# Performance work log

Measured on AMD Instinct MI355X. Metric: run time of the kernel, lower is better.

Reference implementation:

```python
import jax, jax.numpy as jnp
import numpy as np

B, S, RNN, ATTH = 256, 196, 1024, 512  # batch, att_size, rnn_size, att_h_size


def setup_inputs() -> dict:
    key = jax.random.key(0)
    k1, k2, k3, k4, k5, k6, k7 = jax.random.split(key, 7)
    h = jax.random.normal(k1, (B, RNN), dtype=jnp.float32)
    att_feats = jax.random.normal(k2, (B, S, RNN), dtype=jnp.float32)
    p_att_feats = jax.random.normal(k3, (B, S, ATTH), dtype=jnp.float32)
    # learned params (torch nn.Linear: y = x @ W.T + b)
    w_h2att = jax.random.normal(k4, (ATTH, RNN), dtype=jnp.float32) / np.sqrt(RNN)
    b_h2att = jax.random.normal(k5, (ATTH,), dtype=jnp.float32) * 0.01
    w_alpha = jax.random.normal(k6, (1, ATTH), dtype=jnp.float32) / np.sqrt(ATTH)
    b_alpha = jax.random.normal(k7, (1,), dtype=jnp.float32) * 0.01
    return {
        "h": h,
        "att_feats": att_feats,
        "p_att_feats": p_att_feats,
        "w_h2att": w_h2att,
        "b_h2att": b_h2att,
        "w_alpha": w_alpha,
        "b_alpha": b_alpha,
    }


def reference(h, att_feats, p_att_feats, w_h2att, b_h2att, w_alpha, b_alpha):
    # att_h = h2att(h): [B, ATTH]
    att_h = h @ w_h2att.T + b_h2att
    # additive combine + tanh: [B, S, ATTH]
    dot = jnp.tanh(p_att_feats + att_h[:, None, :])
    # alpha_net: [B, S]
    scores = jnp.einsum("bsa,a->bs", dot, w_alpha[0]) + b_alpha[0]
    weight = jax.nn.softmax(scores, axis=1)
    # weighted sum of att_feats: [B, RNN]
    att_res = jnp.einsum("bs,bsd->bd", weight, att_feats)
    return att_res
```

## Files before the change

### kernel.cpp

```cpp
#include <hip/hip_runtime.h>
#include <cstddef>

static constexpr int kB    = 256;
static constexpr int kS    = 196;
static constexpr int kRNN  = 1024;
static constexpr int kATTH = 512;

__device__ __forceinline__ float fast_tanh(float x) {
    x = fminf(12.0f, fmaxf(-12.0f, x));
    float e = __expf(2.0f * x);
    return __fdividef(e - 1.0f, e + 1.0f);
}

__global__ __launch_bounds__(256) void gemm_atth(
    const float* __restrict__ h, const float* __restrict__ w,
    const float* __restrict__ bias, float* __restrict__ att_h) {
    __shared__ float As[32][33];
    __shared__ float Bs[32][33];
    const int bm = blockIdx.x * 32;
    const int bn = blockIdx.y * 32;
    const int tid = threadIdx.x;
    const int lrow = tid >> 3;
    const int lcol = (tid & 7) << 2;
    const int tx = tid & 31;
    const int ty = tid >> 5;
    float acc[4] = {0.f, 0.f, 0.f, 0.f};
    for (int k0 = 0; k0 < kRNN; k0 += 32) {
        float4 av = *(const float4*)&h[(size_t)(bm + lrow) * kRNN + k0 + lcol];
        float4 bv = *(const float4*)&w[(size_t)(bn + lrow) * kRNN + k0 + lcol];
        As[lrow][lcol + 0] = av.x; As[lrow][lcol + 1] = av.y;
        As[lrow][lcol + 2] = av.z; As[lrow][lcol + 3] = av.w;
        Bs[lrow][lcol + 0] = bv.x; Bs[lrow][lcol + 1] = bv.y;
        Bs[lrow][lcol + 2] = bv.z; Bs[lrow][lcol + 3] = bv.w;
        __syncthreads();
#pragma unroll
        for (int k = 0; k < 32; ++k) {
            float bb = Bs[tx][k];
#pragma unroll
            for (int i = 0; i < 4; ++i) acc[i] += As[ty * 4 + i][k] * bb;
        }
        __syncthreads();
    }
    const float bval = bias[bn + tx];
#pragma unroll
    for (int i = 0; i < 4; ++i)
        att_h[(size_t)(bm + ty * 4 + i) * kATTH + bn + tx] = acc[i] + bval;
}

__global__ __launch_bounds__(1024) void att_fused(
    const float* __restrict__ att_feats, const float* __restrict__ p_att,
    const float* __restrict__ att_h, const float* __restrict__ w_alpha,
    const float* __restrict__ b_alpha, float* __restrict__ out) {
    const int b = blockIdx.x;
    const int tid = threadIdx.x;
    const int lane = tid & 63;
    const int wave = tid >> 6;

    __shared__ float sScore[kS];
    __shared__ float4 sRed[3][256];

    const int col = lane << 3;
    const float4 ah0 = *(const float4*)&att_h[(size_t)b * kATTH + col];
    const float4 ah1 = *(const float4*)&att_h[(size_t)b * kATTH + col + 4];
    const float4 wa0 = *(const float4*)&w_alpha[col];
    const float4 wa1 = *(const float4*)&w_alpha[col + 4];
    const float balpha = b_alpha[0];

    for (int s = wave; s < kS; s += 16) {
        const float* p = &p_att[((size_t)b * kS + s) * kATTH + col];
        const float4 p0 = *(const float4*)p;
        const float4 p1 = *(const float4*)(p + 4);
        float partial;
        partial  = fast_tanh(p0.x + ah0.x) * wa0.x;
        partial += fast_tanh(p0.y + ah0.y) * wa0.y;
        partial += fast_tanh(p0.z + ah0.z) * wa0.z;
        partial += fast_tanh(p0.w + ah0.w) * wa0.w;
        partial += fast_tanh(p1.x + ah1.x) * wa1.x;
        partial += fast_tanh(p1.y + ah1.y) * wa1.y;
        partial += fast_tanh(p1.z + ah1.z) * wa1.z;
        partial += fast_tanh(p1.w + ah1.w) * wa1.w;
#pragma unroll
        for (int off = 32; off > 0; off >>= 1)
            partial += __shfl_xor(partial, off, 64);
        if (lane == 0) sScore[s] = partial + balpha;
    }
    __syncthreads();

    if (tid < 64) {
        float vals[4];
        int cnt = 0;
        float m = -3.0e38f;
        for (int s = tid; s < kS; s += 64) {
            vals[cnt] = sScore[s];
            m = fmaxf(m, vals[cnt]);
            ++cnt;
        }
#pragma unroll
        for (int off = 32; off > 0; off >>= 1) m = fmaxf(m, __shfl_xor(m, off, 64));
        float sum = 0.f;
        for (int i = 0; i < cnt; ++i) { vals[i] = __expf(vals[i] - m); sum += vals[i]; }
#pragma unroll
        for (int off = 32; off > 0; off >>= 1) sum += __shfl_xor(sum, off, 64);
        const float inv = __fdividef(1.0f, sum);
        cnt = 0;
        for (int s = tid; s < kS; s += 64) { sScore[s] = vals[cnt] * inv; ++cnt; }
    }
    __syncthreads();

    const int d4 = tid & 255;
    const int sg = tid >> 8;
    float4 acc = {0.f, 0.f, 0.f, 0.f};
    for (int s = sg; s < kS; s += 4) {
        const float ws = sScore[s];
        const float4 v =
            *(const float4*)&att_feats[((size_t)b * kS + s) * kRNN + (d4 << 2)];
        acc.x += ws * v.x; acc.y += ws * v.y;
        acc.z += ws * v.z; acc.w += ws * v.w;
    }
    if (sg > 0) sRed[sg - 1][d4] = acc;
    __syncthreads();
    if (sg == 0) {
        const float4 r0 = sRed[0][d4];
        const float4 r1 = sRed[1][d4];
        const float4 r2 = sRed[2][d4];
        acc.x += r0.x + r1.x + r2.x;
        acc.y += r0.y + r1.y + r2.y;
        acc.z += r0.z + r1.z + r2.z;
        acc.w += r0.w + r1.w + r2.w;
        *(float4*)&out[(size_t)b * kRNN + (d4 << 2)] = acc;
    }
}

extern "C" void kernel_launch(void* const* d_in, const int* in_sizes, int n_in,
                              void* d_out, int out_size, void* d_ws, size_t ws_size,
                              hipStream_t stream) {
    const float* h         = (const float*)d_in[0];
    const float* att_feats = (const float*)d_in[1];
    const float* p_att     = (const float*)d_in[2];
    const float* w_h2att   = (const float*)d_in[3];
    const float* b_h2att   = (const float*)d_in[4];
    const float* w_alpha   = (const float*)d_in[5];
    const float* b_alpha   = (const float*)d_in[6];
    float* out = (float*)d_out;
    float* att_h = (float*)d_ws;

    dim3 g1(kB / 32, kATTH / 32);
    gemm_atth<<<g1, 256, 0, stream>>>(h, w_h2att, b_h2att, att_h);
    att_fused<<<kB, 1024, 0, stream>>>(att_feats, p_att, att_h, w_alpha, b_alpha, out);
}
```

Before: 427.0 us.

## Split fused attention into chunked score, weighted-sum, and reduce kernels

Result: no change. 434.6 us (+1.8%).

```diff
diff --git a/kernel.cpp b/kernel.cpp
--- a/kernel.cpp
+++ b/kernel.cpp
@@ -5,6 +5,8 @@
 static constexpr int kS    = 196;
 static constexpr int kRNN  = 1024;
 static constexpr int kATTH = 512;
+static constexpr int kChunks    = 4;
+static constexpr int kSPerChunk = 49;
 
 __device__ __forceinline__ float fast_tanh(float x) {
     x = fminf(12.0f, fmaxf(-12.0f, x));
@@ -47,88 +49,98 @@
         att_h[(size_t)(bm + ty * 4 + i) * kATTH + bn + tx] = acc[i] + bval;
 }
 
-__global__ __launch_bounds__(1024) void att_fused(
-    const float* __restrict__ att_feats, const float* __restrict__ p_att,
-    const float* __restrict__ att_h, const float* __restrict__ w_alpha,
-    const float* __restrict__ b_alpha, float* __restrict__ out) {
+__global__ __launch_bounds__(256) void scores_kernel(
+    const float* __restrict__ p_att, const float* __restrict__ att_h,
+    const float* __restrict__ w_alpha, float* __restrict__ scores) {
     const int b = blockIdx.x;
+    const int c = blockIdx.y;
+    const int tid = threadIdx.x;
+    const int lane = tid & 63;
+    const int wave = tid >> 6;
+    const int col = lane << 3;
+
+    const float4 ah0 = *(const float4*)&att_h[(size_t)b * kATTH + col];
+    const float4 ah1 = *(const float4*)&att_h[(size_t)b * kATTH + col + 4];
+    const float4 wa0 = *(const float4*)&w_alpha[col];
+    const float4 wa1 = *(const float4*)&w_alpha[col + 4];
+
+    const int s_end = (c + 1) * kSPerChunk;
+    for (int s = c * kSPerChunk + wave; s < s_end; s += 4) {
+        const float* p = &p_att[((size_t)b * kS + s) * kATTH + col];
+        const float4 p0 = *(const float4*)p;
+        const float4 p1 = *(const float4*)(p + 4);
+        float r;
+        r  = fast_tanh(p0.x + ah0.x) * wa0.x;
+        r += fast_tanh(p0.y + ah0.y) * wa0.y;
+        r += fast_tanh(p0.z + ah0.z) * wa0.z;
+        r += fast_tanh(p0.w + ah0.w) * wa0.w;
+        r += fast_tanh(p1.x + ah1.x) * wa1.x;
+        r += fast_tanh(p1.y + ah1.y) * wa1.y;
+        r += fast_tanh(p1.z + ah1.z) * wa1.z;
+        r += fast_tanh(p1.w + ah1.w) * wa1.w;
+#pragma unroll
+        for (int off = 32; off > 0; off >>= 1) r += __shfl_xor(r, off, 64);
+        if (lane == 0) scores[b * kS + s] = r;
+    }
+}
+
+__global__ __launch_bounds__(256) void wsum_kernel(
+    const float* __restrict__ att_feats, const float* __restrict__ scores,
+    float* __restrict__ partial) {
+    const int b = blockIdx.x;
+    const int c = blockIdx.y;
     const int tid = threadIdx.x;
     const int lane = tid & 63;
     const int wave = tid >> 6;
 
-    __shared__ float sScore[kS];
-    __shared__ float4 sRed[3][256];
+    __shared__ float sW[kS];
+    __shared__ float sRed[8];
 
-    const int col = lane << 3;
-    const float4 ah0 = *(const float4*)&att_h[(size_t)b * kATTH + col];
-    const float4 ah1 = *(const float4*)&att_h[(size_t)b * kATTH + col + 4];
-    const float4 wa0 = *(const float4*)&w_alpha[col];
-    const float4 wa1 = *(const float4*)&w_alpha[col + 4];
-    const float balpha = b_alpha[0];
-
-    for (int s = wave; s < kS; s += 16) {
-        const float* p = &p_att[((size_t)b * kS + s) * kATTH + col];
-        const float4 p0 = *(const float4*)p;
-        const float4 p1 = *(const float4*)(p + 4);
-        float partial;
-        partial  = fast_tanh(p0.x + ah0.x) * wa0.x;
-        partial += fast_tanh(p0.y + ah0.y) * wa0.y;
-        partial += fast_tanh(p0.z + ah0.z) * wa0.z;
-        partial += fast_tanh(p0.w + ah0.w) * wa0.w;
-        partial += fast_tanh(p1.x + ah1.x) * wa1.x;
-        partial += fast_tanh(p1.y + ah1.y) * wa1.y;
-        partial += fast_tanh(p1.z + ah1.z) * wa1.z;
-        partial += fast_tanh(p1.w + ah1.w) * wa1.w;
+    const float v = (tid < kS) ? scores[b * kS + tid] : -3.0e38f;
+    float m = v;
 #pragma unroll
-        for (int off = 32; off > 0; off >>= 1)
-            partial += __shfl_xor(partial, off, 64);
-        if (lane == 0) sScore[s] = partial + balpha;
-    }
+    for (int off = 32; off > 0; off >>= 1) m = fmaxf(m, __shfl_xor(m, off, 64));
+    if (lane == 0) sRed[wave] = m;
+    __syncthreads();
+    m = fmaxf(fmaxf(sRed[0], sRed[1]), fmaxf(sRed[2], sRed[3]));
+    const float e = (tid < kS) ? __expf(v - m) : 0.f;
+    float sum = e;
+#pragma unroll
+    for (int off = 32; off > 0; off >>= 1) sum += __shfl_xor(sum, off, 64);
+    if (lane == 0) sRed[4 + wave] = sum;
+    __syncthreads();
+    const float tot = sRed[4] + sRed[5] + sRed[6] + sRed[7];
+    if (tid < kS) sW[tid] = e * __fdividef(1.0f, tot);
     __syncthreads();
 
-    if (tid < 64) {
-        float vals[4];
-        int cnt = 0;
-        float m = -3.0e38f;
-        for (int s = tid; s < kS; s += 64) {
-            vals[cnt] = sScore[s];
-            m = fmaxf(m, vals[cnt]);
-            ++cnt;
-        }
-#pragma unroll
-        for (int off = 32; off > 0; off >>= 1) m = fmaxf(m, __shfl_xor(m, off, 64));
-        float sum = 0.f;
-        for (int i = 0; i < cnt; ++i) { vals[i] = __expf(vals[i] - m); sum += vals[i]; }
-#pragma unroll
-        for (int off = 32; off > 0; off >>= 1) sum += __shfl_xor(sum, off, 64);
-        const float inv = __fdividef(1.0f, sum);
-        cnt = 0;
-        for (int s = tid; s < kS; s += 64) { sScore[s] = vals[cnt] * inv; ++cnt; }
+    const int d4 = tid << 2;
+    const float* base = &att_feats[((size_t)b * kS + c * kSPerChunk) * kRNN + d4];
+    float4 acc = {0.f, 0.f, 0.f, 0.f};
+#pragma unroll 7
+    for (int i = 0; i < kSPerChunk; ++i) {
+        const float w = sW[c * kSPerChunk + i];
+        const float4 x = *(const float4*)(base + (size_t)i * kRNN);
+        acc.x += w * x.x; acc.y += w * x.y;
+        acc.z += w * x.z; acc.w += w * x.w;
     }
-    __syncthreads();
+    *(float4*)&partial[((size_t)b * kChunks + c) * kRNN + d4] = acc;
+}
 
-    const int d4 = tid & 255;
-    const int sg = tid >> 8;
-    float4 acc = {0.f, 0.f, 0.f, 0.f};
-    for (int s = sg; s < kS; s += 4) {
-        const float ws = sScore[s];
-        const float4 v =
-            *(const float4*)&att_feats[((size_t)b * kS + s) * kRNN + (d4 << 2)];
-        acc.x += ws * v.x; acc.y += ws * v.y;
-        acc.z += ws * v.z; acc.w += ws * v.w;
-    }
-    if (sg > 0) sRed[sg - 1][d4] = acc;
-    __syncthreads();
-    if (sg == 0) {
-        const float4 r0 = sRed[0][d4];
-        const float4 r1 = sRed[1][d4];
-        const float4 r2 = sRed[2][d4];
-        acc.x += r0.x + r1.x + r2.x;
-        acc.y += r0.y + r1.y + r2.y;
-        acc.z += r0.z + r1.z + r2.z;
-        acc.w += r0.w + r1.w + r2.w;
-        *(float4*)&out[(size_t)b * kRNN + (d4 << 2)] = acc;
-    }
+__global__ __launch_bounds__(256) void reduce_kernel(
+    const float* __restrict__ partial, float* __restrict__ out) {
+    const int b = blockIdx.x;
+    const int d4 = threadIdx.x << 2;
+    const size_t base = (size_t)b * kChunks * kRNN + d4;
+    const float4 p0 = *(const float4*)&partial[base];
+    const float4 p1 = *(const float4*)&partial[base + kRNN];
+    const float4 p2 = *(const float4*)&partial[base + 2 * kRNN];
+    const float4 p3 = *(const float4*)&partial[base + 3 * kRNN];
+    float4 r;
+    r.x = (p0.x + p1.x) + (p2.x + p3.x);
+    r.y = (p0.y + p1.y) + (p2.y + p3.y);
+    r.z = (p0.z + p1.z) + (p2.z + p3.z);
+    r.w = (p0.w + p1.w) + (p2.w + p3.w);
+    *(float4*)&out[(size_t)b * kRNN + d4] = r;
 }
 
 extern "C" void kernel_launch(void* const* d_in, const int* in_sizes, int n_in,
@@ -140,11 +152,18 @@
     const float* w_h2att   = (const float*)d_in[3];
     const float* b_h2att   = (const float*)d_in[4];
     const float* w_alpha   = (const float*)d_in[5];
-    const float* b_alpha   = (const float*)d_in[6];
     float* out = (float*)d_out;
-    float* att_h = (float*)d_ws;
+
+    char* ws = (char*)d_ws;
+    float* att_h   = (float*)(ws);
+    float* scores  = (float*)(ws + (512u << 10));
+    float* partial = (float*)(ws + (1u << 20));
 
     dim3 g1(kB / 32, kATTH / 32);
     gemm_atth<<<g1, 256, 0, stream>>>(h, w_h2att, b_h2att, att_h);
-    att_fused<<<kB, 1024, 0, stream>>>(att_feats, p_att, att_h, w_alpha, b_alpha, out);
+
+    dim3 g2(kB, kChunks);
+    scores_kernel<<<g2, 256, 0, stream>>>(p_att, att_h, w_alpha, scores);
+    wsum_kernel<<<g2, 256, 0, stream>>>(att_feats, scores, partial);
+    reduce_kernel<<<kB, 256, 0, stream>>>(partial, out);
 }
```
